# Kernel tuning notes

Measured on AMD Instinct MI355X. Metric: run time of the kernel, lower is better.

## Reference

```python
import math
import jax, jax.numpy as jnp
import numpy as np

B, T, C = 1, 4096, 2048
H, HKV, D = 16, 4, 128
ROPE_DIM = 128
ROPE_BASE = 500000.0
RMS_EPS = 1e-05
CHUNK = 2048
FFN_H = 8192


def rmsnorm(x, w, eps=RMS_EPS):
    var = jnp.mean(x * x, axis=-1, keepdims=True)
    return x * jax.lax.rsqrt(var + eps) * w


def rope_apply(q, k, rd=ROPE_DIM, base=ROPE_BASE):
    # q, k: [B, H, T, D]; rotate the first rd dims with interleaved pairs.
    b, h, t, d = q.shape
    rd = min(rd, d)
    inv_freq = 1.0 / (base ** (jnp.arange(0, rd, 2, dtype=jnp.float32) / rd))
    pos = jnp.arange(t, dtype=jnp.float32)
    freqs = pos[:, None] * inv_freq[None, :]              # [T, rd//2]
    cos = jnp.cos(freqs)[None, None]                      # [1,1,T,rd//2]
    sin = jnp.sin(freqs)[None, None]

    def _apply(x):
        x1 = x[..., :rd].reshape(b, x.shape[1], t, rd // 2, 2)
        a, bb = x1[..., 0], x1[..., 1]
        a2 = a * cos - bb * sin
        b3 = a * sin + bb * cos
        y1 = jnp.stack([a2, b3], axis=-1).reshape(b, x.shape[1], t, rd)
        return jnp.concatenate([y1, x[..., rd:]], axis=-1)

    return _apply(q), _apply(k)


def chunked_attention(q, k, v, attn_bias, chunk_size=CHUNK):
    # q,k,v: [B,H,T,D]; attn_bias broadcastable to [B,H,T,T].
    b, h, t, d = q.shape
    scale = 1.0 / math.sqrt(d)
    nc = t // chunk_size
    # [nc, B, H, cs, D]
    qc = q.reshape(b, h, nc, chunk_size, d).transpose(2, 0, 1, 3, 4)
    bias = jnp.broadcast_to(attn_bias, attn_bias.shape[:2] + (t, t))
    bc = bias.reshape(bias.shape[0], bias.shape[1], nc, chunk_size, t).transpose(2, 0, 1, 3, 4)

    def one_chunk(args):
        qs, bs = args
        s = jnp.einsum('bhqd,bhkd->bhqk', qs, k) * scale + bs
        p = jax.nn.softmax(s.astype(jnp.float32), axis=-1).astype(q.dtype)
        return jnp.einsum('bhqk,bhkd->bhqd', p, v)

    oc = jax.lax.map(one_chunk, (qc, bc))                 # [nc,B,H,cs,D]
    return oc.transpose(1, 2, 0, 3, 4).reshape(b, h, t, d)


def l4_block(x, attn_bias, attn_norm_w, wq, wk, wv, wo,
             ffn_norm_w, w_gate, w_up, w_down):
    b, t, c = x.shape
    h = rmsnorm(x, attn_norm_w)
    q = (h @ wq.T).reshape(b, t, H, D).transpose(0, 2, 1, 3)    # [B,H,T,D]
    k = (h @ wk.T).reshape(b, t, HKV, D).transpose(0, 2, 1, 3)  # [B,HKV,T,D]
    v = (h @ wv.T).reshape(b, t, HKV, D).transpose(0, 2, 1, 3)
    q, k = rope_apply(q, k)
    rep = H // HKV
    k = jnp.repeat(k, rep, axis=1)                              # GQA expand
    v = jnp.repeat(v, rep, axis=1)
    y = chunked_attention(q, k, v, attn_bias)
    y = y.transpose(0, 2, 1, 3).reshape(b, t, H * D)
    x = x + y @ wo.T
    h2 = rmsnorm(x, ffn_norm_w)
    ffn = (jax.nn.silu(h2 @ w_gate.T) * (h2 @ w_up.T)) @ w_down.T
    return x + ffn


def setup_inputs() -> dict:
    key = jax.random.key(0)
    ks = jax.random.split(key, 9)
    std = 0.02
    x = jax.random.normal(ks[0], (B, T, C), dtype=jnp.float32)
    causal = jnp.triu(jnp.ones((T, T), dtype=bool), k=1)
    attn_bias = jnp.where(causal, jnp.float32(-1e9), jnp.float32(0.0))[None, None]
    return {
        'x': x,
        'attn_bias': attn_bias,
        'attn_norm_w': jnp.ones((C,), jnp.float32),
        'wq': jax.random.normal(ks[1], (H * D, C), jnp.float32) * std,
        'wk': jax.random.normal(ks[2], (HKV * D, C), jnp.float32) * std,
        'wv': jax.random.normal(ks[3], (HKV * D, C), jnp.float32) * std,
        'wo': jax.random.normal(ks[4], (C, H * D), jnp.float32) * std,
        'ffn_norm_w': jnp.ones((C,), jnp.float32),
        'w_gate': jax.random.normal(ks[5], (FFN_H, C), jnp.float32) * std,
        'w_up': jax.random.normal(ks[6], (FFN_H, C), jnp.float32) * std,
        'w_down': jax.random.normal(ks[7], (C, FFN_H), jnp.float32) * std,
    }


def reference(x, attn_bias, attn_norm_w, wq, wk, wv, wo,
              ffn_norm_w, w_gate, w_up, w_down):
    return l4_block(x, attn_bias, attn_norm_w, wq, wk, wv, wo,
                    ffn_norm_w, w_gate, w_up, w_down)
```

## Files before the change

kernel.cpp:

```cpp
#include <hip/hip_runtime.h>
#include <math.h>

#define DEVI static __device__ __forceinline__

typedef __attribute__((ext_vector_type(8))) short bf16x8;
typedef __attribute__((ext_vector_type(4))) short bf16x4;
typedef __attribute__((ext_vector_type(8))) unsigned short ushort8;
typedef __attribute__((ext_vector_type(4))) unsigned short us4;
typedef __attribute__((ext_vector_type(4))) float f32x4;

DEVI unsigned short f32_bf16(float f) {
  unsigned int u = __float_as_uint(f);
  u += 0x7fffu + ((u >> 16) & 1u);
  return (unsigned short)(u >> 16);
}
DEVI float bf16_f32(unsigned short h) {
  return __uint_as_float(((unsigned int)h) << 16);
}

DEVI void async16(void* lds, const void* g) {
  __builtin_amdgcn_global_load_lds(
      (const __attribute__((address_space(1))) void*)g,
      (__attribute__((address_space(3))) void*)lds,
      16, 0, 0);
}

#if __has_builtin(__builtin_amdgcn_mfma_f32_16x16x16bf16_1k)
DEVI f32x4 mfma16(bf16x4 a, bf16x4 b, f32x4 c) {
  return __builtin_amdgcn_mfma_f32_16x16x16bf16_1k(a, b, c, 0, 0, 0);
}
#else
DEVI f32x4 mfma16(bf16x4 a, bf16x4 b, f32x4 c) {
  asm volatile("v_mfma_f32_16x16x16_bf16 %0, %1, %2, %0" : "+v"(c) : "v"(a), "v"(b));
  return c;
}
#endif

__global__ __launch_bounds__(256) void cast_bf16_kernel(
    const float* __restrict__ src, unsigned short* __restrict__ dst, long n8) {
  long i = (long)blockIdx.x * 256 + threadIdx.x;
  if (i >= n8) return;
  const float4 a = *(const float4*)(src + i * 8);
  const float4 b = *(const float4*)(src + i * 8 + 4);
  ushort8 o;
  o[0] = f32_bf16(a.x); o[1] = f32_bf16(a.y); o[2] = f32_bf16(a.z); o[3] = f32_bf16(a.w);
  o[4] = f32_bf16(b.x); o[5] = f32_bf16(b.y); o[6] = f32_bf16(b.z); o[7] = f32_bf16(b.w);
  *(ushort8*)(dst + i * 8) = o;
}

__global__ __launch_bounds__(256) void cast_gu_kernel(
    const float* __restrict__ gate, const float* __restrict__ up,
    unsigned short* __restrict__ dst) {
  long i = (long)blockIdx.x * 256 + threadIdx.x;
  long row = i >> 8;
  long col = (i & 255) * 8;
  const float* src = ((row & 1) ? up : gate) + ((row >> 1) << 11) + col;
  const float4 a = *(const float4*)(src);
  const float4 b = *(const float4*)(src + 4);
  ushort8 o;
  o[0] = f32_bf16(a.x); o[1] = f32_bf16(a.y); o[2] = f32_bf16(a.z); o[3] = f32_bf16(a.w);
  o[4] = f32_bf16(b.x); o[5] = f32_bf16(b.y); o[6] = f32_bf16(b.z); o[7] = f32_bf16(b.w);
  *(ushort8*)(dst + i * 8) = o;
}

__global__ __launch_bounds__(256) void rope_table_kernel(float2* __restrict__ tab) {
  int idx = blockIdx.x * 256 + threadIdx.x;
  int t = idx >> 6, i = idx & 63;
  float inv = __expf(-(float)(2 * i) * (1.0f / 128.0f) * 13.122363377404328f);
  float f = (float)t * inv;
  tab[idx] = make_float2(cosf(f), sinf(f));
}

__global__ __launch_bounds__(256) void rope_apply_kernel(
    unsigned short* __restrict__ qkv, const float2* __restrict__ tab) {
  const int row = blockIdx.x;
  const int tid = threadIdx.x;
#pragma unroll
  for (int it = 0; it < 5; ++it) {
    int p = tid + it * 256;
    int head = p >> 6, i = p & 63;
    int col = (p < 1024) ? (head * 128 + 2 * i) : (2048 + (head - 16) * 128 + 2 * i);
    unsigned short* ptr = qkv + (long)row * 3072 + col;
    float a = bf16_f32(ptr[0]), b = bf16_f32(ptr[1]);
    float2 cs = tab[row * 64 + i];
    float a2 = a * cs.x - b * cs.y;
    float b2 = a * cs.y + b * cs.x;
    ptr[0] = f32_bf16(a2);
    ptr[1] = f32_bf16(b2);
  }
}

__global__ __launch_bounds__(256) void rmsnorm_kernel(
    const float* __restrict__ x, const float* __restrict__ wgt,
    unsigned short* __restrict__ out) {
  __shared__ float red[4];
  const int row = blockIdx.x;
  const int tid = threadIdx.x;
  const float* xr = x + (long)row * 2048 + tid * 8;
  const float4 v0 = *(const float4*)(xr);
  const float4 v1 = *(const float4*)(xr + 4);
  float ss = v0.x * v0.x + v0.y * v0.y + v0.z * v0.z + v0.w * v0.w +
             v1.x * v1.x + v1.y * v1.y + v1.z * v1.z + v1.w * v1.w;
#pragma unroll
  for (int off = 1; off < 64; off <<= 1) ss += __shfl_xor(ss, off);
  if ((tid & 63) == 0) red[tid >> 6] = ss;
  __syncthreads();
  float tot = red[0] + red[1] + red[2] + red[3];
  float sc = rsqrtf(tot * (1.0f / 2048.0f) + 1e-5f);
  const float4 w0 = *(const float4*)(wgt + tid * 8);
  const float4 w1 = *(const float4*)(wgt + tid * 8 + 4);
  ushort8 o;
  o[0] = f32_bf16(v0.x * sc * w0.x); o[1] = f32_bf16(v0.y * sc * w0.y);
  o[2] = f32_bf16(v0.z * sc * w0.z); o[3] = f32_bf16(v0.w * sc * w0.w);
  o[4] = f32_bf16(v1.x * sc * w1.x); o[5] = f32_bf16(v1.y * sc * w1.y);
  o[6] = f32_bf16(v1.z * sc * w1.z); o[7] = f32_bf16(v1.w * sc * w1.w);
  *(ushort8*)(out + (long)row * 2048 + tid * 8) = o;
}

template <int BN, int EPI>
__global__ __launch_bounds__(512, 2) void gemm_p(
    const unsigned short* __restrict__ A, const unsigned short* __restrict__ B,
    void* __restrict__ Cout, const float* __restrict__ res, int M, int N, int K) {
  constexpr int MH = (BN == 256) ? 2 : 1;
  constexpr int MF = MH * 4;
  constexpr int BL = (BN == 256) ? 2 : 1;
  __shared__ __align__(16) unsigned short As[4][256 * 32];
  __shared__ __align__(16) unsigned short Bs[4][BN * 32];

  const int tid = threadIdx.x;
  const int lane = tid & 63;
  const int w = tid >> 6;
  const int c = lane & 15, g = lane >> 4;
  const int wm = (BN == 256) ? (w >> 2) * 128 : (w >> 1) * 64;
  const int wn = (BN == 256) ? (w & 3) * 64 : (w & 1) * 64;
  const int gs = ((g ^ ((c >> 1) & 3)) << 3);

  const int id = blockIdx.y * gridDim.x + blockIdx.x;
  const int cpx = (gridDim.x * gridDim.y) >> 3;
  const int sid = (id & 7) * cpx + (id >> 3);
  const int bx = sid % gridDim.x;
  const int by = sid / gridDim.x;
  const long m0 = (long)bx * 256;
  const long n0 = (long)by * BN;

  const f32x4 fzero = {0.f, 0.f, 0.f, 0.f};
  f32x4 acc[MF][4];
#pragma unroll
  for (int i = 0; i < MF; ++i)
#pragma unroll
    for (int j = 0; j < 4; ++j) acc[i][j] = fzero;

  auto stageA = [&](int buf, int k0) {
#pragma unroll
    for (int q = 0; q < 2; ++q) {
      int G = q * 512 + tid;
      int sg = (G & 3) ^ ((G >> 3) & 3);
      async16(&As[buf][(q * 512 + (tid & ~63)) * 8],
              A + (m0 + (G >> 2)) * (long)K + k0 + sg * 8);
    }
  };
  auto stageB = [&](int buf, int k0) {
#pragma unroll
    for (int q = 0; q < BL; ++q) {
      int G = q * 512 + tid;
      int sg = (G & 3) ^ ((G >> 3) & 3);
      async16(&Bs[buf][(q * 512 + (tid & ~63)) * 8],
              B + (n0 + (G >> 2)) * (long)K + k0 + sg * 8);
    }
  };

  const int NT = K >> 5;
  stageA(0, 0);
  stageB(0, 0);
  stageA(1, 32);
  stageB(1, 32);
  if constexpr (BN == 256)
    asm volatile("s_waitcnt vmcnt(4)" ::: "memory");
  else
    asm volatile("s_waitcnt vmcnt(3)" ::: "memory");
  __builtin_amdgcn_s_barrier();

  for (int t = 0; t < NT; ++t) {
    const int buf = t & 3;
    const unsigned short* Ab = As[buf];
    const unsigned short* Bb = Bs[buf];
    const bool pf = (t + 2 < NT);
    const int nb = (t + 2) & 3;

    bf16x8 bfr[4];
#pragma unroll
    for (int nf = 0; nf < 4; ++nf)
      bfr[nf] = *(const bf16x8*)(Bb + (wn + nf * 16 + c) * 32 + gs);

#pragma unroll
    for (int mh = 0; mh < MH; ++mh) {
      bf16x8 af[4];
#pragma unroll
      for (int mf = 0; mf < 4; ++mf)
        af[mf] = *(const bf16x8*)(Ab + (wm + mh * 64 + mf * 16 + c) * 32 + gs);
      if (pf) {
        if (mh == 0) stageA(nb, (t + 2) << 5);
        if (mh == MH - 1) stageB(nb, (t + 2) << 5);
      }
      __builtin_amdgcn_sched_barrier(0);
      __builtin_amdgcn_s_setprio(1);
#pragma unroll
      for (int mf = 0; mf < 4; ++mf)
#pragma unroll
        for (int nf = 0; nf < 4; ++nf)
          acc[mh * 4 + mf][nf] = __builtin_amdgcn_mfma_f32_16x16x32_bf16(
              af[mf], bfr[nf], acc[mh * 4 + mf][nf], 0, 0, 0);
      __builtin_amdgcn_s_setprio(0);
    }

    if (pf) {
      if constexpr (BN == 256)
        asm volatile("s_waitcnt vmcnt(4)" ::: "memory");
      else
        asm volatile("s_waitcnt vmcnt(3)" ::: "memory");
    } else {
      asm volatile("s_waitcnt vmcnt(0)" ::: "memory");
    }
    __builtin_amdgcn_s_barrier();
  }

#pragma unroll
  for (int i = 0; i < MF; ++i) {
#pragma unroll
    for (int j = 0; j < 4; ++j) {
      const long row0 = m0 + wm + i * 16 + g * 4;
      const long col = n0 + wn + j * 16 + c;
#pragma unroll
      for (int r = 0; r < 4; ++r) {
        float v = acc[i][j][r];
        if (EPI == 0) {
          ((unsigned short*)Cout)[(row0 + r) * N + col] = f32_bf16(v);
        } else if (EPI == 1) {
          ((float*)Cout)[(row0 + r) * N + col] = res[(row0 + r) * N + col] + v;
        } else {
          float other = __shfl_xor(v, 1);
          if (!(c & 1)) {
            float sg2 = v / (1.0f + __expf(-v));
            ((unsigned short*)Cout)[(row0 + r) * (long)(N >> 1) + (col >> 1)] =
                f32_bf16(sg2 * other);
          }
        }
      }
    }
  }
}

__global__ __launch_bounds__(256) void transpose_v(
    const unsigned short* __restrict__ qkv, unsigned short* __restrict__ vT) {
  __shared__ __align__(16) unsigned short tile[64][72];
  const int tx = blockIdx.x;
  const int dx = blockIdx.y;
  const int tid = threadIdx.x;
  const int r = tid >> 3, cg = tid & 7;
#pragma unroll
  for (int it = 0; it < 2; ++it) {
    const unsigned short* src =
        qkv + (long)(tx * 64 + r + it * 32) * 3072 + 2560 + dx * 64 + cg * 8;
    *(ushort8*)(&tile[r + it * 32][cg * 8]) = *(const ushort8*)src;
  }
  __syncthreads();
#pragma unroll
  for (int it = 0; it < 2; ++it) {
    int d = r + it * 32;
    ushort8 v;
#pragma unroll
    for (int j = 0; j < 8; ++j) v[j] = tile[cg * 8 + j][d];
    *(ushort8*)(vT + (long)(dx * 64 + d) * 4096 + tx * 64 + cg * 8) = v;
  }
}

__global__ __launch_bounds__(512, 2) void attn_kernel(
    const unsigned short* __restrict__ qkv, const unsigned short* __restrict__ vT,
    unsigned short* __restrict__ y) {
  constexpr float SCL = 0.08838834764831845f * 1.4426950408889634f;
  __shared__ __align__(16) unsigned short Kb[2][64 * 128];
  __shared__ __align__(16) unsigned short Vb[2][128 * 64];

  const int tid = threadIdx.x;
  const int lane = tid & 63;
  const int w = tid >> 6;
  const int c = lane & 15, g = lane >> 4;
  const int h = blockIdx.x >> 4;
  const int pid = blockIdx.x & 15;
  const int kvh = h >> 2;
  const int qt = (w < 4) ? pid : (31 - pid);
  const int q0w = qt * 128 + (w & 3) * 32;
  const int nsteps = 2 * (31 - pid) + 2;

  const f32x4 fzero = {0.f, 0.f, 0.f, 0.f};

  bf16x8 qf[2][4];
#pragma unroll
  for (int mt = 0; mt < 2; ++mt)
#pragma unroll
    for (int kk = 0; kk < 4; ++kk)
      qf[mt][kk] = *(const bf16x8*)(qkv + (long)(q0w + mt * 16 + c) * 3072 +
                                    h * 128 + kk * 32 + g * 8);

  f32x4 o[2][8];
#pragma unroll
  for (int mt = 0; mt < 2; ++mt)
#pragma unroll
    for (int dt = 0; dt < 8; ++dt) o[mt][dt] = fzero;
  float m[2] = {-1e30f, -1e30f}, l[2] = {0.f, 0.f};

  auto stage = [&](int buf, int kv0) {
#pragma unroll
    for (int k = 0; k < 2; ++k) {
      int G = k * 512 + tid;
      int row = G >> 4, colg = (G & 15) ^ (row & 7);
      async16(&Kb[buf][(k * 512 + (tid & ~63)) * 8],
              qkv + (long)(kv0 + row) * 3072 + 2048 + kvh * 128 + colg * 8);
    }
#pragma unroll
    for (int k = 0; k < 2; ++k) {
      int G = k * 512 + tid;
      int row = G >> 3, colg = (G & 7) ^ (row & 7);
      async16(&Vb[buf][(k * 512 + (tid & ~63)) * 8],
              vT + (long)(kvh * 128 + row) * 4096 + kv0 + colg * 8);
    }
  };

  stage(0, 0);
  for (int s = 0; s < nsteps; ++s) {
    const int kv0 = s * 64;
    const int bi = s & 1;
    if (s + 1 < nsteps) {
      stage(bi ^ 1, kv0 + 64);
      asm volatile("s_waitcnt vmcnt(4)" ::: "memory");
    } else {
      asm volatile("s_waitcnt vmcnt(0)" ::: "memory");
    }
    __builtin_amdgcn_s_barrier();
    if (kv0 <= q0w + 31) {
      const unsigned short* Ks = Kb[bi];
      const unsigned short* Vs = Vb[bi];
      f32x4 sv[2][4];
#pragma unroll
      for (int mt = 0; mt < 2; ++mt)
#pragma unroll
        for (int nt = 0; nt < 4; ++nt) sv[mt][nt] = fzero;
#pragma unroll
      for (int kk = 0; kk < 4; ++kk) {
        bf16x8 kf[4];
#pragma unroll
        for (int nt = 0; nt < 4; ++nt)
          kf[nt] = *(const bf16x8*)(Ks + (nt * 16 + c) * 128 +
                                    (((kk * 4 + g) ^ (c & 7)) << 3));
#pragma unroll
        for (int mt = 0; mt < 2; ++mt)
#pragma unroll
          for (int nt = 0; nt < 4; ++nt)
            sv[mt][nt] = __builtin_amdgcn_mfma_f32_16x16x32_bf16(
                kf[nt], qf[mt][kk], sv[mt][nt], 0, 0, 0);
      }
      const bool need_mask = (kv0 + 63 > q0w);
      float al[2];
#pragma unroll
      for (int mt = 0; mt < 2; ++mt) {
        const int qrow = q0w + mt * 16 + c;
#pragma unroll
        for (int nt = 0; nt < 4; ++nt)
#pragma unroll
          for (int r = 0; r < 4; ++r) {
            float xx = sv[mt][nt][r] * SCL;
            if (need_mask && (kv0 + nt * 16 + g * 4 + r > qrow)) xx = -3.0e38f;
            sv[mt][nt][r] = xx;
          }
        float mx = -3.0e38f;
#pragma unroll
        for (int nt = 0; nt < 4; ++nt)
#pragma unroll
          for (int r = 0; r < 4; ++r) mx = fmaxf(mx, sv[mt][nt][r]);
        mx = fmaxf(mx, __shfl_xor(mx, 16));
        mx = fmaxf(mx, __shfl_xor(mx, 32));
        const float mn = fmaxf(m[mt], mx);
        const float a = exp2f(m[mt] - mn);
        m[mt] = mn;
        al[mt] = a;
        float rs = 0.f;
#pragma unroll
        for (int nt = 0; nt < 4; ++nt)
#pragma unroll
          for (int r = 0; r < 4; ++r) {
            float p = exp2f(sv[mt][nt][r] - mn);
            sv[mt][nt][r] = p;
            rs += p;
          }
        rs += __shfl_xor(rs, 16);
        rs += __shfl_xor(rs, 32);
        l[mt] = l[mt] * a + rs;
#pragma unroll
        for (int dt = 0; dt < 8; ++dt) o[mt][dt] *= al[mt];
      }
#pragma unroll
      for (int nt = 0; nt < 4; ++nt) {
        bf16x4 pb[2];
#pragma unroll
        for (int mt = 0; mt < 2; ++mt) {
          int lo_, hi_;
          float s0 = sv[mt][nt][0], s1 = sv[mt][nt][1];
          float s2 = sv[mt][nt][2], s3 = sv[mt][nt][3];
          asm("v_cvt_pk_bf16_f32 %0, %1, %2" : "=v"(lo_) : "v"(s0), "v"(s1));
          asm("v_cvt_pk_bf16_f32 %0, %1, %2" : "=v"(hi_) : "v"(s2), "v"(s3));
          int2 pk = make_int2(lo_, hi_);
          pb[mt] = __builtin_bit_cast(bf16x4, pk);
        }
#pragma unroll
        for (int dt = 0; dt < 8; ++dt) {
          bf16x4 vt = *(const bf16x4*)(Vs + (dt * 16 + c) * 64 +
                                       (((nt * 2 + (g >> 1)) ^ (c & 7)) << 3) +
                                       (g & 1) * 4);
          o[0][dt] = mfma16(vt, pb[0], o[0][dt]);
          o[1][dt] = mfma16(vt, pb[1], o[1][dt]);
        }
      }
    }
    __builtin_amdgcn_s_barrier();
  }
#pragma unroll
  for (int mt = 0; mt < 2; ++mt) {
    const float inv = 1.0f / l[mt];
    const long qrow = q0w + mt * 16 + c;
#pragma unroll
    for (int dt = 0; dt < 8; ++dt) {
      us4 st;
      st[0] = f32_bf16(o[mt][dt][0] * inv);
      st[1] = f32_bf16(o[mt][dt][1] * inv);
      st[2] = f32_bf16(o[mt][dt][2] * inv);
      st[3] = f32_bf16(o[mt][dt][3] * inv);
      *(us4*)(y + qrow * 2048 + h * 128 + dt * 16 + g * 4) = st;
    }
  }
}

extern "C" void kernel_launch(void* const* d_in, const int* in_sizes, int n_in,
                              void* d_out, int out_size, void* d_ws, size_t ws_size,
                              hipStream_t stream) {
  (void)in_sizes; (void)n_in; (void)out_size; (void)ws_size;
  const float* x      = (const float*)d_in[0];
  const float* attn_w = (const float*)d_in[2];
  const float* wq     = (const float*)d_in[3];
  const float* wk     = (const float*)d_in[4];
  const float* wv     = (const float*)d_in[5];
  const float* wo     = (const float*)d_in[6];
  const float* ffn_w  = (const float*)d_in[7];
  const float* wg     = (const float*)d_in[8];
  const float* wu     = (const float*)d_in[9];
  const float* wd     = (const float*)d_in[10];
  float* out = (float*)d_out;

  char* ws = (char*)d_ws;
  size_t off = 0;
  auto alloc = [&](size_t bytes) {
    char* p = ws + off;
    off += (bytes + 255) & ~(size_t)255;
    return p;
  };
  float2* rope_tab        = (float2*)alloc(4096UL * 64 * sizeof(float2));
  unsigned short* wqkv_b  = (unsigned short*)alloc(3072UL * 2048 * 2);
  unsigned short* wo_b    = (unsigned short*)alloc(2048UL * 2048 * 2);
  unsigned short* wgu_b   = (unsigned short*)alloc(16384UL * 2048 * 2);
  unsigned short* wd_b    = (unsigned short*)alloc(2048UL * 8192 * 2);
  unsigned short* h_b     = (unsigned short*)alloc(4096UL * 2048 * 2);
  unsigned short* qkv_b   = (unsigned short*)alloc(4096UL * 3072 * 2);
  unsigned short* vT_b    = (unsigned short*)alloc(512UL * 4096 * 2);
  unsigned short* y_b     = (unsigned short*)alloc(4096UL * 2048 * 2);
  float* r1               = (float*)alloc(4096UL * 2048 * 4);
  unsigned short* t_b     = (unsigned short*)alloc(4096UL * 8192 * 2);

  cast_bf16_kernel<<<2048, 256, 0, stream>>>(wq, wqkv_b, 524288);
  cast_bf16_kernel<<<512, 256, 0, stream>>>(wk, wqkv_b + 2048L * 2048, 131072);
  cast_bf16_kernel<<<512, 256, 0, stream>>>(wv, wqkv_b + 2560L * 2048, 131072);
  cast_bf16_kernel<<<2048, 256, 0, stream>>>(wo, wo_b, 524288);
  cast_gu_kernel<<<16384, 256, 0, stream>>>(wg, wu, wgu_b);
  cast_bf16_kernel<<<8192, 256, 0, stream>>>(wd, wd_b, 2097152);
  rope_table_kernel<<<1024, 256, 0, stream>>>(rope_tab);

  rmsnorm_kernel<<<4096, 256, 0, stream>>>(x, attn_w, h_b);
  {
    dim3 grid(16, 12);
    gemm_p<256, 0><<<grid, 512, 0, stream>>>(h_b, wqkv_b, qkv_b, nullptr, 4096, 3072, 2048);
  }
  rope_apply_kernel<<<4096, 256, 0, stream>>>(qkv_b, rope_tab);
  {
    dim3 grid(64, 8);
    transpose_v<<<grid, 256, 0, stream>>>(qkv_b, vT_b);
  }
  attn_kernel<<<256, 512, 0, stream>>>(qkv_b, vT_b, y_b);
  {
    dim3 grid(16, 16);
    gemm_p<128, 1><<<grid, 512, 0, stream>>>(y_b, wo_b, r1, x, 4096, 2048, 2048);
  }

  rmsnorm_kernel<<<4096, 256, 0, stream>>>(r1, ffn_w, h_b);
  {
    dim3 grid(16, 64);
    gemm_p<256, 2><<<grid, 512, 0, stream>>>(h_b, wgu_b, t_b, nullptr, 4096, 16384, 2048);
  }
  {
    dim3 grid(16, 16);
    gemm_p<128, 1><<<grid, 512, 0, stream>>>(t_b, wd_b, out, r1, 4096, 2048, 8192);
  }
}
```

Baseline: 887.3 us.

## Add 256x256 split-half GEMM with interleaved async staging for QKV and gate/up

Adds a new GEMM kernel, gemm_dp, that splits each 256x256 tile into A and B halves of 128 rows each with a K step of 64. It double-buffers those halves and issues the next stage's half-tile global-to-LDS loads between the four MFMA quadrant phases. Work-group ids are remapped across 8 groups for locality, and MFMA sections run at raised wave priority. It replaces the previous gemm_p for the QKV and fused gate/up projections, aiming to hide memory latency behind compute. The cost is more barriers per iteration and a more intricate vmcnt accounting that must stay correct.

```diff
diff --git a/kernel.cpp b/kernel.cpp
--- a/kernel.cpp
+++ b/kernel.cpp
@@ -115,6 +115,203 @@
   o[4] = f32_bf16(v1.x * sc * w1.x); o[5] = f32_bf16(v1.y * sc * w1.y);
   o[6] = f32_bf16(v1.z * sc * w1.z); o[7] = f32_bf16(v1.w * sc * w1.w);
   *(ushort8*)(out + (long)row * 2048 + tid * 8) = o;
+}
+
+template <int EPI>
+__global__ __launch_bounds__(512, 2) void gemm_dp(
+    const unsigned short* __restrict__ A, const unsigned short* __restrict__ B,
+    void* __restrict__ Cout, const float* __restrict__ res, int M, int N, int K) {
+  __shared__ __align__(16) unsigned short As[2][2][128 * 64];
+  __shared__ __align__(16) unsigned short Bs[2][2][128 * 64];
+
+  const int tid = threadIdx.x;
+  const int lane = tid & 63;
+  const int w = tid >> 6;
+  const int c = lane & 15, g = lane >> 4;
+  const int a_grp = w >> 2;
+  const int b_grp = w & 3;
+  const int sw0 = ((g ^ (c & 7)) << 3);
+  const int sw1 = (((4 + g) ^ (c & 7)) << 3);
+
+  const int id = blockIdx.y * gridDim.x + blockIdx.x;
+  const int cpx = (gridDim.x * gridDim.y) >> 3;
+  const int sid = (id & 7) * cpx + (id >> 3);
+  const int bx = sid % gridDim.x;
+  const int by = sid / gridDim.x;
+  const long m0 = (long)bx * 256;
+  const long n0 = (long)by * 256;
+
+  const f32x4 fzero = {0.f, 0.f, 0.f, 0.f};
+  f32x4 acc[2][4][2][2];
+#pragma unroll
+  for (int qm = 0; qm < 2; ++qm)
+#pragma unroll
+    for (int mf = 0; mf < 4; ++mf)
+#pragma unroll
+      for (int qn = 0; qn < 2; ++qn)
+#pragma unroll
+        for (int nf = 0; nf < 2; ++nf) acc[qm][mf][qn][nf] = fzero;
+
+  auto stageAh = [&](int bufi, int h, int k0) {
+#pragma unroll
+    for (int q = 0; q < 2; ++q) {
+      int G = q * 512 + tid;
+      int ks = (G & 7) ^ ((G >> 3) & 7);
+      async16(&As[bufi][h][(q * 512 + (tid & ~63)) * 8],
+              A + (m0 + h * 128 + (G >> 3)) * (long)K + k0 + ks * 8);
+    }
+  };
+  auto stageBh = [&](int bufi, int h, int k0) {
+#pragma unroll
+    for (int q = 0; q < 2; ++q) {
+      int G = q * 512 + tid;
+      int ks = (G & 7) ^ ((G >> 3) & 7);
+      async16(&Bs[bufi][h][(q * 512 + (tid & ~63)) * 8],
+              B + (n0 + h * 128 + (G >> 3)) * (long)K + k0 + ks * 8);
+    }
+  };
+
+  const int NT = K >> 6;
+  stageAh(0, 0, 0);
+  stageBh(0, 0, 0);
+  stageBh(0, 1, 0);
+  stageAh(0, 1, 0);
+  stageAh(1, 0, 64);
+  stageBh(1, 0, 64);
+  asm volatile("s_waitcnt vmcnt(6)" ::: "memory");
+  __builtin_amdgcn_s_barrier();
+
+  bf16x8 af[4][2];
+  bf16x8 bfr[2][2][2];
+
+  for (int t = 0; t < NT; ++t) {
+    const int buf = t & 1;
+    const int nbuf = buf ^ 1;
+    const int k1 = (t + 1) << 6;
+    const int k2 = (t + 2) << 6;
+    const bool s1 = (t + 1 < NT), s2 = (t + 2 < NT);
+
+#pragma unroll
+    for (int mf = 0; mf < 4; ++mf) {
+      const int row = a_grp * 64 + mf * 16 + c;
+      af[mf][0] = *(const bf16x8*)(As[buf][0] + row * 64 + sw0);
+      af[mf][1] = *(const bf16x8*)(As[buf][0] + row * 64 + sw1);
+    }
+#pragma unroll
+    for (int nf = 0; nf < 2; ++nf) {
+      const int row = b_grp * 32 + nf * 16 + c;
+      bfr[0][nf][0] = *(const bf16x8*)(Bs[buf][0] + row * 64 + sw0);
+      bfr[0][nf][1] = *(const bf16x8*)(Bs[buf][0] + row * 64 + sw1);
+    }
+    if (s1) stageBh(nbuf, 1, k1);
+    __builtin_amdgcn_s_barrier();
+    asm volatile("s_waitcnt lgkmcnt(0)" ::: "memory");
+    __builtin_amdgcn_sched_barrier(0);
+    __builtin_amdgcn_s_setprio(1);
+#pragma unroll
+    for (int kk = 0; kk < 2; ++kk)
+#pragma unroll
+      for (int mf = 0; mf < 4; ++mf)
+#pragma unroll
+        for (int nf = 0; nf < 2; ++nf)
+          acc[0][mf][0][nf] = __builtin_amdgcn_mfma_f32_16x16x32_bf16(
+              af[mf][kk], bfr[0][nf][kk], acc[0][mf][0][nf], 0, 0, 0);
+    __builtin_amdgcn_s_setprio(0);
+    __builtin_amdgcn_s_barrier();
+
+#pragma unroll
+    for (int nf = 0; nf < 2; ++nf) {
+      const int row = b_grp * 32 + nf * 16 + c;
+      bfr[1][nf][0] = *(const bf16x8*)(Bs[buf][1] + row * 64 + sw0);
+      bfr[1][nf][1] = *(const bf16x8*)(Bs[buf][1] + row * 64 + sw1);
+    }
+    if (s1) stageAh(nbuf, 1, k1);
+    __builtin_amdgcn_s_barrier();
+    asm volatile("s_waitcnt lgkmcnt(0)" ::: "memory");
+    __builtin_amdgcn_sched_barrier(0);
+    __builtin_amdgcn_s_setprio(1);
+#pragma unroll
+    for (int kk = 0; kk < 2; ++kk)
+#pragma unroll
+      for (int mf = 0; mf < 4; ++mf)
+#pragma unroll
+        for (int nf = 0; nf < 2; ++nf)
+          acc[0][mf][1][nf] = __builtin_amdgcn_mfma_f32_16x16x32_bf16(
+              af[mf][kk], bfr[1][nf][kk], acc[0][mf][1][nf], 0, 0, 0);
+    __builtin_amdgcn_s_setprio(0);
+    if (s1) asm volatile("s_waitcnt vmcnt(6)" ::: "memory");
+    __builtin_amdgcn_s_barrier();
+
+#pragma unroll
+    for (int mf = 0; mf < 4; ++mf) {
+      const int row = a_grp * 64 + mf * 16 + c;
+      af[mf][0] = *(const bf16x8*)(As[buf][1] + row * 64 + sw0);
+      af[mf][1] = *(const bf16x8*)(As[buf][1] + row * 64 + sw1);
+    }
+    if (s2) stageAh(buf, 0, k2);
+    __builtin_amdgcn_s_barrier();
+    asm volatile("s_waitcnt lgkmcnt(0)" ::: "memory");
+    __builtin_amdgcn_sched_barrier(0);
+    __builtin_amdgcn_s_setprio(1);
+#pragma unroll
+    for (int kk = 0; kk < 2; ++kk)
+#pragma unroll
+      for (int mf = 0; mf < 4; ++mf)
+#pragma unroll
+        for (int nf = 0; nf < 2; ++nf)
+          acc[1][mf][0][nf] = __builtin_amdgcn_mfma_f32_16x16x32_bf16(
+              af[mf][kk], bfr[0][nf][kk], acc[1][mf][0][nf], 0, 0, 0);
+    __builtin_amdgcn_s_setprio(0);
+    __builtin_amdgcn_s_barrier();
+
+    if (s2) stageBh(buf, 0, k2);
+    __builtin_amdgcn_s_setprio(1);
+#pragma unroll
+    for (int kk = 0; kk < 2; ++kk)
+#pragma unroll
+      for (int mf = 0; mf < 4; ++mf)
+#pragma unroll
+        for (int nf = 0; nf < 2; ++nf)
+          acc[1][mf][1][nf] = __builtin_amdgcn_mfma_f32_16x16x32_bf16(
+              af[mf][kk], bfr[1][nf][kk], acc[1][mf][1][nf], 0, 0, 0);
+    __builtin_amdgcn_s_setprio(0);
+    if (s2)
+      asm volatile("s_waitcnt vmcnt(6)" ::: "memory");
+    else if (s1)
+      asm volatile("s_waitcnt vmcnt(0)" ::: "memory");
+    __builtin_amdgcn_s_barrier();
+  }
+
+#pragma unroll
+  for (int qm = 0; qm < 2; ++qm) {
+#pragma unroll
+    for (int mf = 0; mf < 4; ++mf) {
+#pragma unroll
+      for (int qn = 0; qn < 2; ++qn) {
+#pragma unroll
+        for (int nf = 0; nf < 2; ++nf) {
+          const long row0 = m0 + qm * 128 + a_grp * 64 + mf * 16 + g * 4;
+          const long col = n0 + qn * 128 + b_grp * 32 + nf * 16 + c;
+#pragma unroll
+          for (int r = 0; r < 4; ++r) {
+            float v = acc[qm][mf][qn][nf][r];
+            if (EPI == 0) {
+              ((unsigned short*)Cout)[(row0 + r) * N + col] = f32_bf16(v);
+            } else if (EPI == 1) {
+              ((float*)Cout)[(row0 + r) * N + col] = res[(row0 + r) * N + col] + v;
+            } else {
+              float other = __shfl_xor(v, 1);
+              if (!(c & 1)) {
+                float sg = v / (1.0f + __expf(-v));
+                ((unsigned short*)Cout)[(row0 + r) * (long)(N >> 1) + (col >> 1)] =
+                    f32_bf16(sg * other);
+              }
+            }
+          }
+        }
+      }
+    }
+  }
 }
 
 template <int BN, int EPI>
@@ -485,7 +682,7 @@
   rmsnorm_kernel<<<4096, 256, 0, stream>>>(x, attn_w, h_b);
   {
     dim3 grid(16, 12);
-    gemm_p<256, 0><<<grid, 512, 0, stream>>>(h_b, wqkv_b, qkv_b, nullptr, 4096, 3072, 2048);
+    gemm_dp<0><<<grid, 512, 0, stream>>>(h_b, wqkv_b, qkv_b, nullptr, 4096, 3072, 2048);
   }
   rope_apply_kernel<<<4096, 256, 0, stream>>>(qkv_b, rope_tab);
   {
@@ -501,7 +698,7 @@
   rmsnorm_kernel<<<4096, 256, 0, stream>>>(r1, ffn_w, h_b);
   {
     dim3 grid(16, 64);
-    gemm_p<256, 2><<<grid, 512, 0, stream>>>(h_b, wgu_b, t_b, nullptr, 4096, 16384, 2048);
+    gemm_dp<2><<<grid, 512, 0, stream>>>(h_b, wgu_b, t_b, nullptr, 4096, 16384, 2048);
   }
   {
     dim3 grid(16, 16);
```

Measured after the change: 895.6 us. Within noise of the previous version (+0.9%).

## Use single-buffered 128x128 GEMM with XCD-aware block swizzle for QKV and gate-up

Applied to the files above, without the earlier changes.

Adds a new GEMM kernel with 128x128 tiles, 256 threads, BK=64, an XOR-swizzled LDS layout and a block-id remap that spreads consecutive tiles across 8 groups (XCD-aware scheduling). The QKV and gate/up projections now use it instead of the 4-stage pipelined 256-wide kernel. The intent is higher occupancy (4 blocks per CU) and better L2 locality, traded against losing the multi-stage async prefetch pipeline, since each k-step waits for its loads to finish.

```diff
diff --git a/kernel.cpp b/kernel.cpp
--- a/kernel.cpp
+++ b/kernel.cpp
@@ -115,6 +115,103 @@
   o[4] = f32_bf16(v1.x * sc * w1.x); o[5] = f32_bf16(v1.y * sc * w1.y);
   o[6] = f32_bf16(v1.z * sc * w1.z); o[7] = f32_bf16(v1.w * sc * w1.w);
   *(ushort8*)(out + (long)row * 2048 + tid * 8) = o;
+}
+
+template <int EPI>
+__global__ __launch_bounds__(256, 4) void gemm97(
+    const unsigned short* __restrict__ A, const unsigned short* __restrict__ B,
+    void* __restrict__ Cout, const float* __restrict__ res, int M, int N, int K) {
+  __shared__ __align__(16) unsigned short As[128 * 64];
+  __shared__ __align__(16) unsigned short Bs[128 * 64];
+
+  const int tid = threadIdx.x;
+  const int lane = tid & 63;
+  const int w = tid >> 6;
+  const int c = lane & 15, g = lane >> 4;
+  const int wm = (w >> 1) * 64, wn = (w & 1) * 64;
+  const int c7 = c & 7;
+
+  const int id = blockIdx.y * gridDim.x + blockIdx.x;
+  const int cpx = (gridDim.x * gridDim.y) >> 3;
+  const int sid = (id & 7) * cpx + (id >> 3);
+  const int bx = sid % gridDim.x;
+  const int by = sid / gridDim.x;
+  const long m0 = (long)bx * 128;
+  const long n0 = (long)by * 128;
+
+  const f32x4 fzero = {0.f, 0.f, 0.f, 0.f};
+  f32x4 acc[4][4];
+#pragma unroll
+  for (int i = 0; i < 4; ++i)
+#pragma unroll
+    for (int j = 0; j < 4; ++j) acc[i][j] = fzero;
+
+  const int NT = K >> 6;
+  for (int t = 0; t < NT; ++t) {
+    const int k0 = t << 6;
+    __builtin_amdgcn_s_barrier();
+#pragma unroll
+    for (int q = 0; q < 4; ++q) {
+      int G = q * 256 + tid;
+      int row = G >> 3;
+      int ks = (G & 7) ^ (row & 7);
+      async16(&As[(q * 256 + (tid & ~63)) * 8], A + (m0 + row) * (long)K + k0 + ks * 8);
+    }
+#pragma unroll
+    for (int q = 0; q < 4; ++q) {
+      int G = q * 256 + tid;
+      int row = G >> 3;
+      int ks = (G & 7) ^ (row & 7);
+      async16(&Bs[(q * 256 + (tid & ~63)) * 8], B + (n0 + row) * (long)K + k0 + ks * 8);
+    }
+    asm volatile("s_waitcnt vmcnt(0)" ::: "memory");
+    __builtin_amdgcn_s_barrier();
+
+#pragma unroll
+    for (int kk = 0; kk < 2; ++kk) {
+      const int sw = (((kk * 4 + g) ^ c7) << 3);
+      bf16x8 af[4], bf[4];
+#pragma unroll
+      for (int mf = 0; mf < 4; ++mf)
+        af[mf] = *(const bf16x8*)(As + (wm + mf * 16 + c) * 64 + sw);
+#pragma unroll
+      for (int nf = 0; nf < 4; ++nf)
+        bf[nf] = *(const bf16x8*)(Bs + (wn + nf * 16 + c) * 64 + sw);
+      __builtin_amdgcn_s_setprio(1);
+#pragma unroll
+      for (int mf = 0; mf < 4; ++mf)
+#pragma unroll
+        for (int nf = 0; nf < 4; ++nf)
+          acc[mf][nf] = __builtin_amdgcn_mfma_f32_16x16x32_bf16(
+              af[mf], bf[nf], acc[mf][nf], 0, 0, 0);
+      __builtin_amdgcn_s_setprio(0);
+    }
+  }
+
+#pragma unroll
+  for (int i = 0; i < 4; ++i) {
+#pragma unroll
+    for (int j = 0; j < 4; ++j) {
+      const long row0 = m0 + wm + i * 16 + g * 4;
+      const long col = n0 + wn + j * 16 + c;
+#pragma unroll
+      for (int r = 0; r < 4; ++r) {
+        float v = acc[i][j][r];
+        if (EPI == 0) {
+          ((unsigned short*)Cout)[(row0 + r) * N + col] = f32_bf16(v);
+        } else if (EPI == 1) {
+          ((float*)Cout)[(row0 + r) * N + col] = res[(row0 + r) * N + col] + v;
+        } else {
+          float other = __shfl_xor(v, 1);
+          if (!(c & 1)) {
+            float sg = v / (1.0f + __expf(-v));
+            ((unsigned short*)Cout)[(row0 + r) * (long)(N >> 1) + (col >> 1)] =
+                f32_bf16(sg * other);
+          }
+        }
+      }
+    }
+  }
 }
 
 template <int BN, int EPI>
@@ -484,8 +581,8 @@
 
   rmsnorm_kernel<<<4096, 256, 0, stream>>>(x, attn_w, h_b);
   {
-    dim3 grid(16, 12);
-    gemm_p<256, 0><<<grid, 512, 0, stream>>>(h_b, wqkv_b, qkv_b, nullptr, 4096, 3072, 2048);
+    dim3 grid(32, 24);
+    gemm97<0><<<grid, 256, 0, stream>>>(h_b, wqkv_b, qkv_b, nullptr, 4096, 3072, 2048);
   }
   rope_apply_kernel<<<4096, 256, 0, stream>>>(qkv_b, rope_tab);
   {
@@ -500,8 +597,8 @@
 
   rmsnorm_kernel<<<4096, 256, 0, stream>>>(r1, ffn_w, h_b);
   {
-    dim3 grid(16, 64);
-    gemm_p<256, 2><<<grid, 512, 0, stream>>>(h_b, wgu_b, t_b, nullptr, 4096, 16384, 2048);
+    dim3 grid(32, 128);
+    gemm97<2><<<grid, 256, 0, stream>>>(h_b, wgu_b, t_b, nullptr, 4096, 16384, 2048);
   }
   {
     dim3 grid(16, 16);
```

Result: no change. 900.5 us (+1.5%).
